# Kernel tuning notes

Measured on AMD Instinct MI355X. Metric: run time of the kernel, lower is better.

Reference implementation:

```python
import jax, jax.numpy as jnp
import numpy as np

N_HEADS, D_MODEL, D_HEAD = 16, 1024, 64
BATCH, SEQ = 2, 2048
INIT_RANGE = 0.02


def setup_inputs() -> dict:
    key = jax.random.key(0)
    ks = jax.random.split(key, 5)
    x = jax.random.normal(ks[0], (BATCH, SEQ, D_MODEL), dtype=jnp.float32)
    W_Q = jax.random.normal(ks[1], (N_HEADS, D_MODEL, D_HEAD), dtype=jnp.float32) * INIT_RANGE
    W_K = jax.random.normal(ks[2], (N_HEADS, D_MODEL, D_HEAD), dtype=jnp.float32) * INIT_RANGE
    W_V = jax.random.normal(ks[3], (N_HEADS, D_MODEL, D_HEAD), dtype=jnp.float32) * INIT_RANGE
    W_O = jax.random.normal(ks[4], (N_HEADS, D_HEAD, D_MODEL), dtype=jnp.float32) * INIT_RANGE
    b_Q = jnp.zeros((N_HEADS, D_HEAD), dtype=jnp.float32)
    b_K = jnp.zeros((N_HEADS, D_HEAD), dtype=jnp.float32)
    b_V = jnp.zeros((N_HEADS, D_HEAD), dtype=jnp.float32)
    b_O = jnp.zeros((D_MODEL,), dtype=jnp.float32)
    return {"normalized_resid_pre": x, "W_Q": W_Q, "W_K": W_K, "W_V": W_V,
            "W_O": W_O, "b_Q": b_Q, "b_K": b_K, "b_V": b_V, "b_O": b_O}


def reference(normalized_resid_pre, W_Q, W_K, W_V, W_O, b_Q, b_K, b_V, b_O):
    x = normalized_resid_pre  # [b, s, d_model]
    q = jnp.einsum('bsm,hmd->bshd', x, W_Q) + b_Q  # [b, s, h, d_head]
    k = jnp.einsum('bsm,hmd->bshd', x, W_K) + b_K
    v = jnp.einsum('bsm,hmd->bshd', x, W_V) + b_V
    scores = jnp.einsum('bqhd,bkhd->bhqk', q, k) / jnp.sqrt(jnp.float32(D_HEAD))
    seq = x.shape[1]
    causal = jnp.tril(jnp.ones((seq, seq), dtype=bool))  # True where allowed
    scores = jnp.where(causal, scores, jnp.float32(-jnp.inf))
    pattern = jax.nn.softmax(scores, axis=-1)  # [b, h, q, k]
    z = jnp.einsum('bhqk,bkhd->bqhd', pattern, v)
    attn_out = jnp.einsum('bqhd,hdm->bqm', z, W_O) + b_O
    return attn_out
```

## Files before the change

kernel.cpp:

```cpp
#include <hip/hip_runtime.h>
#include <hip/hip_bf16.h>

#define BATCH 2
#define SEQL 2048
#define NH 16
#define DH 64
#define DM 1024
#define LDK 72
#define QSCALE 0.1803368801111244f

typedef __hip_bfloat16 bf16;
typedef __attribute__((ext_vector_type(8))) short  bf16x8;
typedef __attribute__((ext_vector_type(4))) float  f32x4;

__device__ __forceinline__ void gl_lds16(const void* g, void* l) {
    __builtin_amdgcn_global_load_lds(
        (const __attribute__((address_space(1))) unsigned int*)g,
        (__attribute__((address_space(3))) unsigned int*)l, 16, 0, 0);
}

__global__ __launch_bounds__(256) void prep_kernel(
    const float* __restrict__ x,
    const float* __restrict__ Wq, const float* __restrict__ Wk,
    const float* __restrict__ Wv, const float* __restrict__ Wo,
    bf16* __restrict__ Wt, bf16* __restrict__ xb)
{
    const int zi = blockIdx.z;
    if (zi == 4) {
        const int bid = blockIdx.y * 16 + blockIdx.x;
        const size_t base = ((size_t)bid * 256 + threadIdx.x) * 4;
        #pragma unroll
        for (int it = 0; it < 16; ++it) {
            const size_t i = base + (size_t)it * 262144;
            const float4 v = *(const float4*)(x + i);
            bf16 o[4];
            o[0] = __float2bfloat16(v.x); o[1] = __float2bfloat16(v.y);
            o[2] = __float2bfloat16(v.z); o[3] = __float2bfloat16(v.w);
            *(uint2*)(xb + i) = *(const uint2*)o;
        }
        return;
    }

    __shared__ float ts[64][65];
    const float* src = (zi == 0) ? Wq : (zi == 1) ? Wk : (zi == 2) ? Wv : Wo;
    bf16* dst = Wt + (size_t)zi * DM * DM;
    const int row0 = blockIdx.y * 64;
    const int col0 = blockIdx.x * 64;
    const int tx = threadIdx.x & 63;
    const int ty = threadIdx.x >> 6;

    if (zi < 3) {
        const int h = col0 >> 6;
        #pragma unroll
        for (int i = 0; i < 16; ++i) {
            const int r = ty + 4 * i;
            ts[r][tx] = src[h * (DM * DH) + (row0 + r) * DH + tx];
        }
    } else {
        #pragma unroll
        for (int i = 0; i < 16; ++i) {
            const int r = ty + 4 * i;
            ts[r][tx] = src[(size_t)(row0 + r) * DM + col0 + tx];
        }
    }
    __syncthreads();
    #pragma unroll
    for (int i = 0; i < 16; ++i) {
        const int rr = ty + 4 * i;
        dst[(size_t)(col0 + rr) * DM + row0 + tx] = __float2bfloat16(ts[tx][rr]);
    }
}

__global__ __launch_bounds__(256) void qkv_gemm(
    const bf16* __restrict__ xb, const bf16* __restrict__ Wt,
    const float* __restrict__ bq, const float* __restrict__ bk, const float* __restrict__ bv,
    bf16* __restrict__ qkv)
{
    __shared__ __align__(16) bf16 As[2][128 * 32];
    __shared__ __align__(16) bf16 Bs[2][128 * 32];

    const int t = threadIdx.x;
    const int lane = t & 63, w = t >> 6;
    const int ml = lane & 15, quad = lane >> 4;
    const int wr = w >> 1, wc = w & 1;
    const int bn = blockIdx.x, bm = blockIdx.y, which = blockIdx.z;

    const bf16* A0 = xb + (size_t)(bm * 128) * DM;
    const bf16* B0 = Wt + (size_t)which * DM * DM + (size_t)(bn * 128) * DM;
    const float* bias = (which == 0) ? bq : (which == 1) ? bk : bv;
    bf16* outb = qkv + (size_t)which * (BATCH * SEQL * NH * DH);
    const float oscale = (which == 0) ? QSCALE : 1.0f;

    f32x4 acc[4][4];
    #pragma unroll
    for (int i = 0; i < 4; ++i)
        #pragma unroll
        for (int j = 0; j < 4; ++j) acc[i][j] = (f32x4){0.f, 0.f, 0.f, 0.f};

    const int r0 = t >> 2, c0 = (t & 3) * 8;
    const int f1 = t + 256;
    const int r1 = f1 >> 2, c1 = (f1 & 3) * 8;

    for (int kt = 0; kt < DM / 64; ++kt) {
        const int k0 = kt * 64;
        __syncthreads();
        #pragma unroll
        for (int half = 0; half < 2; ++half) {
            const int kh = k0 + half * 32;
            gl_lds16(A0 + (size_t)r0 * DM + kh + c0, &As[half][t * 8]);
            gl_lds16(A0 + (size_t)r1 * DM + kh + c1, &As[half][f1 * 8]);
            gl_lds16(B0 + (size_t)r0 * DM + kh + c0, &Bs[half][t * 8]);
            gl_lds16(B0 + (size_t)r1 * DM + kh + c1, &Bs[half][f1 * 8]);
        }
        __syncthreads();
        #pragma unroll
        for (int half = 0; half < 2; ++half) {
            bf16x8 af[4], bfr[4];
            #pragma unroll
            for (int i = 0; i < 4; ++i)
                af[i] = *(const bf16x8*)&As[half][(wr * 64 + i * 16 + ml) * 32 + quad * 8];
            #pragma unroll
            for (int j = 0; j < 4; ++j)
                bfr[j] = *(const bf16x8*)&Bs[half][(wc * 64 + j * 16 + ml) * 32 + quad * 8];
            #pragma unroll
            for (int i = 0; i < 4; ++i)
                #pragma unroll
                for (int j = 0; j < 4; ++j)
                    acc[i][j] = __builtin_amdgcn_mfma_f32_16x16x32_bf16(af[i], bfr[j], acc[i][j], 0, 0, 0);
        }
    }

    float bb[4];
    #pragma unroll
    for (int j = 0; j < 4; ++j) bb[j] = bias[bn * 128 + wc * 64 + j * 16 + ml];

    if (which == 2) {
        #pragma unroll
        for (int i = 0; i < 4; ++i) {
            const int row0v = bm * 128 + wr * 64 + i * 16 + quad * 4;
            const int b = row0v >> 11;
            const int s0 = row0v & (SEQL - 1);
            #pragma unroll
            for (int j = 0; j < 4; ++j) {
                const int col = bn * 128 + wc * 64 + j * 16 + ml;
                const int h = col >> 6, d = col & 63;
                bf16 tmp[4];
                #pragma unroll
                for (int rg = 0; rg < 4; ++rg)
                    tmp[rg] = __float2bfloat16(acc[i][j][rg] + bb[j]);
                *(uint2*)&outb[(((size_t)(b * NH + h)) * DH + d) * SEQL + s0] =
                    *(const uint2*)tmp;
            }
        }
    } else {
        #pragma unroll
        for (int i = 0; i < 4; ++i) {
            #pragma unroll
            for (int rg = 0; rg < 4; ++rg) {
                const int row = bm * 128 + wr * 64 + i * 16 + quad * 4 + rg;
                const int b = row >> 11;
                const int s = row & (SEQL - 1);
                #pragma unroll
                for (int j = 0; j < 4; ++j) {
                    const int col = bn * 128 + wc * 64 + j * 16 + ml;
                    const int h = col >> 6, d = col & 63;
                    outb[(((size_t)(b * NH + h)) * SEQL + s) * DH + d] =
                        __float2bfloat16((acc[i][j][rg] + bb[j]) * oscale);
                }
            }
        }
    }
}

__global__ __launch_bounds__(256) void oproj_gemm(
    const bf16* __restrict__ zb, const bf16* __restrict__ Bt,
    const float* __restrict__ bo, float* __restrict__ out)
{
    __shared__ __align__(16) bf16 As[2][128 * 32];
    __shared__ __align__(16) bf16 Bs[2][64 * 32];

    const int t = threadIdx.x;
    const int lane = t & 63, w = t >> 6;
    const int ml = lane & 15, quad = lane >> 4;
    const int wr = w >> 1, wc = w & 1;
    const int bn = blockIdx.x, bm = blockIdx.y;

    const bf16* A0 = zb + (size_t)(bm * 128) * DM;
    const bf16* B0 = Bt + (size_t)(bn * 64) * DM;

    f32x4 acc[4][2];
    #pragma unroll
    for (int i = 0; i < 4; ++i)
        #pragma unroll
        for (int j = 0; j < 2; ++j) acc[i][j] = (f32x4){0.f, 0.f, 0.f, 0.f};

    const int r0 = t >> 2, c0 = (t & 3) * 8;
    const int f1 = t + 256;
    const int r1 = f1 >> 2, c1 = (f1 & 3) * 8;

    for (int kt = 0; kt < DM / 64; ++kt) {
        const int k0 = kt * 64;
        __syncthreads();
        #pragma unroll
        for (int half = 0; half < 2; ++half) {
            const int kh = k0 + half * 32;
            gl_lds16(A0 + (size_t)r0 * DM + kh + c0, &As[half][t * 8]);
            gl_lds16(A0 + (size_t)r1 * DM + kh + c1, &As[half][f1 * 8]);
            gl_lds16(B0 + (size_t)r0 * DM + kh + c0, &Bs[half][t * 8]);
        }
        __syncthreads();
        #pragma unroll
        for (int half = 0; half < 2; ++half) {
            bf16x8 af[4], bfr[2];
            #pragma unroll
            for (int i = 0; i < 4; ++i)
                af[i] = *(const bf16x8*)&As[half][(wr * 64 + i * 16 + ml) * 32 + quad * 8];
            #pragma unroll
            for (int j = 0; j < 2; ++j)
                bfr[j] = *(const bf16x8*)&Bs[half][(wc * 32 + j * 16 + ml) * 32 + quad * 8];
            #pragma unroll
            for (int i = 0; i < 4; ++i)
                #pragma unroll
                for (int j = 0; j < 2; ++j)
                    acc[i][j] = __builtin_amdgcn_mfma_f32_16x16x32_bf16(af[i], bfr[j], acc[i][j], 0, 0, 0);
        }
    }

    float bb[2];
    #pragma unroll
    for (int j = 0; j < 2; ++j) bb[j] = bo[bn * 64 + wc * 32 + j * 16 + ml];

    #pragma unroll
    for (int i = 0; i < 4; ++i) {
        #pragma unroll
        for (int rg = 0; rg < 4; ++rg) {
            const int row = bm * 128 + wr * 64 + i * 16 + quad * 4 + rg;
            #pragma unroll
            for (int j = 0; j < 2; ++j) {
                const int col = bn * 64 + wc * 32 + j * 16 + ml;
                out[(size_t)row * DM + col] = acc[i][j][rg] + bb[j];
            }
        }
    }
}

__global__ __launch_bounds__(256) void attn_kernel(
    const bf16* __restrict__ qg, const bf16* __restrict__ kg, const bf16* __restrict__ vtg,
    bf16* __restrict__ z)
{
    __shared__ __align__(16) bf16 KsS[2][64 * 64];
    __shared__ __align__(16) bf16 VtS[2][64 * 64];
    __shared__ bf16 PsS[4][16 * LDK];

    const int t    = threadIdx.x;
    const int lane = t & 63;
    const int w    = t >> 6;
    const int m    = lane & 15;
    const int quad = lane >> 4;

    const int bh = blockIdx.x;
    const int b  = bh >> 4;
    const int h  = bh & 15;
    const int qt = (gridDim.y - 1) - blockIdx.y;
    const int q0 = qt * 64;

    const size_t base   = (size_t)bh * SEQL * DH;
    const size_t vtbase = (size_t)bh * DH * SEQL;

    const int s0 = w * 128 + lane;
    const int s1 = s0 + 64;
    const int r0s = s0 >> 3, c0s = (s0 & 7) ^ (r0s & 7);
    const int r1s = s1 >> 3, c1s = (s1 & 7) ^ (r1s & 7);

    bf16x8 aq[2];
    {
        const bf16* qp = qg + base + (size_t)(q0 + w * 16 + m) * DH + quad * 8;
        aq[0] = *(const bf16x8*)(qp);
        aq[1] = *(const bf16x8*)(qp + 32);
    }

    const short ob = (m == 0) ? (short)0x3F80 : (short)0;
    const bf16x8 bones = {ob, ob, ob, ob, ob, ob, ob, ob};

    f32x4 zacc[4];
    #pragma unroll
    for (int nt = 0; nt < 4; ++nt) zacc[nt] = (f32x4){0.f, 0.f, 0.f, 0.f};
    f32x4 lacc = (f32x4){0.f, 0.f, 0.f, 0.f};

    bf16* Psw = PsS[w];

    {
        gl_lds16(kg + base + (size_t)r0s * DH + c0s * 8, &KsS[0][s0 * 8]);
        gl_lds16(kg + base + (size_t)r1s * DH + c1s * 8, &KsS[0][s1 * 8]);
        gl_lds16(vtg + vtbase + (size_t)r0s * SEQL + c0s * 8, &VtS[0][s0 * 8]);
        gl_lds16(vtg + vtbase + (size_t)r1s * SEQL + c1s * 8, &VtS[0][s1 * 8]);
    }

    for (int kt = 0; kt <= qt; ++kt) {
        const int cur = kt & 1;
        __syncthreads();

        if (kt < qt) {
            const int kc = (kt + 1) * 64;
            bf16* Kd = &KsS[cur ^ 1][0];
            bf16* Vd = &VtS[cur ^ 1][0];
            gl_lds16(kg + base + (size_t)(kc + r0s) * DH + c0s * 8, Kd + s0 * 8);
            gl_lds16(kg + base + (size_t)(kc + r1s) * DH + c1s * 8, Kd + s1 * 8);
            gl_lds16(vtg + vtbase + (size_t)r0s * SEQL + kc + c0s * 8, Vd + s0 * 8);
            gl_lds16(vtg + vtbase + (size_t)r1s * SEQL + kc + c1s * 8, Vd + s1 * 8);
        }

        const bf16* Ks = &KsS[cur][0];
        const bf16* Vt = &VtS[cur][0];

        f32x4 sc[4];
        #pragma unroll
        for (int nt = 0; nt < 4; ++nt) sc[nt] = (f32x4){0.f, 0.f, 0.f, 0.f};
        __builtin_amdgcn_s_setprio(1);
        #pragma unroll
        for (int ks = 0; ks < 2; ++ks) {
            #pragma unroll
            for (int nt = 0; nt < 4; ++nt) {
                const int row = nt * 16 + m;
                const int pc  = ((ks << 2) + quad) ^ (m & 7);
                const bf16x8 bk = *(const bf16x8*)(&Ks[row * 64 + pc * 8]);
                sc[nt] = __builtin_amdgcn_mfma_f32_16x16x32_bf16(aq[ks], bk, sc[nt], 0, 0, 0);
            }
        }
        __builtin_amdgcn_s_setprio(0);
        if (kt == qt) {
            #pragma unroll
            for (int nt = 0; nt < 4; ++nt) {
                const int col = nt * 16 + m;
                #pragma unroll
                for (int rg = 0; rg < 4; ++rg) {
                    const int row = w * 16 + quad * 4 + rg;
                    if (col > row) sc[nt][rg] = -1e30f;
                }
            }
        }

        #pragma unroll
        for (int nt = 0; nt < 4; ++nt)
            #pragma unroll
            for (int rg = 0; rg < 4; ++rg)
                Psw[(quad * 4 + rg) * LDK + nt * 16 + m] =
                    __float2bfloat16(__builtin_exp2f(sc[nt][rg]));

        __builtin_amdgcn_s_setprio(1);
        #pragma unroll
        for (int ks = 0; ks < 2; ++ks) {
            const bf16x8 ap = *(const bf16x8*)(&Psw[m * LDK + ks * 32 + quad * 8]);
            lacc = __builtin_amdgcn_mfma_f32_16x16x32_bf16(ap, bones, lacc, 0, 0, 0);
            #pragma unroll
            for (int nt = 0; nt < 4; ++nt) {
                const int row = nt * 16 + m;
                const int pc  = ((ks << 2) + quad) ^ (m & 7);
                const bf16x8 bv = *(const bf16x8*)(&Vt[row * 64 + pc * 8]);
                zacc[nt] = __builtin_amdgcn_mfma_f32_16x16x32_bf16(ap, bv, zacc[nt], 0, 0, 0);
            }
        }
        __builtin_amdgcn_s_setprio(0);
    }

    float invl[4];
    #pragma unroll
    for (int rg = 0; rg < 4; ++rg)
        invl[rg] = 1.f / __shfl(lacc[rg], quad * 16);
    #pragma unroll
    for (int nt = 0; nt < 4; ++nt) {
        const int d = nt * 16 + m;
        #pragma unroll
        for (int rg = 0; rg < 4; ++rg) {
            const int qrow = q0 + w * 16 + quad * 4 + rg;
            z[(((size_t)b * SEQL + qrow) * NH + h) * DH + d] =
                __float2bfloat16(zacc[nt][rg] * invl[rg]);
        }
    }
}

extern "C" void kernel_launch(void* const* d_in, const int* in_sizes, int n_in,
                              void* d_out, int out_size, void* d_ws, size_t ws_size,
                              hipStream_t stream)
{
    const float* x  = (const float*)d_in[0];
    const float* Wq = (const float*)d_in[1];
    const float* Wk = (const float*)d_in[2];
    const float* Wv = (const float*)d_in[3];
    const float* Wo = (const float*)d_in[4];
    const float* bq = (const float*)d_in[5];
    const float* bk = (const float*)d_in[6];
    const float* bv = (const float*)d_in[7];
    const float* bo = (const float*)d_in[8];
    float* out = (float*)d_out;

    const size_t TOK = (size_t)BATCH * SEQL;
    const size_t QKV = TOK * DM;
    bf16* xb  = (bf16*)d_ws;
    bf16* Wt  = xb + QKV;
    bf16* qkv = Wt + 4 * (size_t)DM * DM;
    bf16* zb  = qkv + 3 * QKV;

    prep_kernel<<<dim3(16, 16, 5), 256, 0, stream>>>(x, Wq, Wk, Wv, Wo, Wt, xb);
    qkv_gemm<<<dim3(8, 32, 3), 256, 0, stream>>>(xb, Wt, bq, bk, bv, qkv);
    attn_kernel<<<dim3(BATCH * NH, SEQL / 64), 256, 0, stream>>>(
        qkv, qkv + QKV, qkv + 2 * QKV, zb);
    oproj_gemm<<<dim3(16, 32), 256, 0, stream>>>(zb, Wt + 3 * (size_t)DM * DM, bo, out);
}
```

Before: 185.1 us.

## Restructure attention to 32x32 MFMA with split-KV warps and register-resident P

Rewrites the attention kernel to use 32x32x16 MFMAs, computing S transposed (K x Q) so the probabilities stay in registers and are exchanged across half-waves with shuffles instead of a round trip through LDS. The four waves now split into two query groups and two KV halves, and the KV-half partial outputs are merged through shared memory at the end. The row sum is accumulated in scalar adds instead of an extra MFMA against a ones vector, and the fully masked diagonal quarter is skipped. This aims to cut LDS traffic and MFMA count, at the cost of an extra reduction step, more registers, and skewed per-wave work on the diagonal tile.

```diff
diff --git a/kernel.cpp b/kernel.cpp
--- a/kernel.cpp
+++ b/kernel.cpp
@@ -6,17 +6,23 @@
 #define NH 16
 #define DH 64
 #define DM 1024
-#define LDK 72
 #define QSCALE 0.1803368801111244f
 
 typedef __hip_bfloat16 bf16;
-typedef __attribute__((ext_vector_type(8))) short  bf16x8;
-typedef __attribute__((ext_vector_type(4))) float  f32x4;
+typedef __attribute__((ext_vector_type(8)))  short bf16x8;
+typedef __attribute__((ext_vector_type(4)))  float f32x4;
+typedef __attribute__((ext_vector_type(16))) float f32x16;
 
 __device__ __forceinline__ void gl_lds16(const void* g, void* l) {
     __builtin_amdgcn_global_load_lds(
         (const __attribute__((address_space(1))) unsigned int*)g,
         (__attribute__((address_space(3))) unsigned int*)l, 16, 0, 0);
+}
+
+__device__ __forceinline__ unsigned int pkbf(float a, float b) {
+    union { bf16 h[2]; unsigned int u; } x;
+    x.h[0] = __float2bfloat16(a); x.h[1] = __float2bfloat16(b);
+    return x.u;
 }
 
 __global__ __launch_bounds__(256) void prep_kernel(
@@ -250,13 +256,14 @@
 {
     __shared__ __align__(16) bf16 KsS[2][64 * 64];
     __shared__ __align__(16) bf16 VtS[2][64 * 64];
-    __shared__ bf16 PsS[4][16 * LDK];
 
     const int t    = threadIdx.x;
     const int lane = t & 63;
     const int w    = t >> 6;
-    const int m    = lane & 15;
-    const int quad = lane >> 4;
+    const int q5   = lane & 31;
+    const int hl   = lane >> 5;
+    const int qgr  = w & 1;
+    const int kvg  = w >> 1;
 
     const int bh = blockIdx.x;
     const int b  = bh >> 4;
@@ -267,34 +274,29 @@
     const size_t base   = (size_t)bh * SEQL * DH;
     const size_t vtbase = (size_t)bh * DH * SEQL;
 
-    const int s0 = w * 128 + lane;
-    const int s1 = s0 + 64;
+    const int s0 = t, s1 = t + 256;
     const int r0s = s0 >> 3, c0s = (s0 & 7) ^ (r0s & 7);
     const int r1s = s1 >> 3, c1s = (s1 & 7) ^ (r1s & 7);
 
-    bf16x8 aq[2];
+    bf16x8 aq[4];
     {
-        const bf16* qp = qg + base + (size_t)(q0 + w * 16 + m) * DH + quad * 8;
-        aq[0] = *(const bf16x8*)(qp);
-        aq[1] = *(const bf16x8*)(qp + 32);
-    }
-
-    const short ob = (m == 0) ? (short)0x3F80 : (short)0;
-    const bf16x8 bones = {ob, ob, ob, ob, ob, ob, ob, ob};
-
-    f32x4 zacc[4];
-    #pragma unroll
-    for (int nt = 0; nt < 4; ++nt) zacc[nt] = (f32x4){0.f, 0.f, 0.f, 0.f};
-    f32x4 lacc = (f32x4){0.f, 0.f, 0.f, 0.f};
-
-    bf16* Psw = PsS[w];
-
-    {
-        gl_lds16(kg + base + (size_t)r0s * DH + c0s * 8, &KsS[0][s0 * 8]);
-        gl_lds16(kg + base + (size_t)r1s * DH + c1s * 8, &KsS[0][s1 * 8]);
-        gl_lds16(vtg + vtbase + (size_t)r0s * SEQL + c0s * 8, &VtS[0][s0 * 8]);
-        gl_lds16(vtg + vtbase + (size_t)r1s * SEQL + c1s * 8, &VtS[0][s1 * 8]);
-    }
+        const bf16* qp = qg + base + (size_t)(q0 + qgr * 32 + q5) * DH;
+        #pragma unroll
+        for (int c = 0; c < 4; ++c)
+            aq[c] = *(const bf16x8*)(qp + c * 16 + hl * 8);
+    }
+
+    f32x16 zacc[2];
+    #pragma unroll
+    for (int dg = 0; dg < 2; ++dg)
+        #pragma unroll
+        for (int r = 0; r < 16; ++r) zacc[dg][r] = 0.f;
+    float lacc = 0.f;
+
+    gl_lds16(kg + base + (size_t)r0s * DH + c0s * 8, &KsS[0][s0 * 8]);
+    gl_lds16(kg + base + (size_t)r1s * DH + c1s * 8, &KsS[0][s1 * 8]);
+    gl_lds16(vtg + vtbase + (size_t)r0s * SEQL + c0s * 8, &VtS[0][s0 * 8]);
+    gl_lds16(vtg + vtbase + (size_t)r1s * SEQL + c1s * 8, &VtS[0][s1 * 8]);
 
     for (int kt = 0; kt <= qt; ++kt) {
         const int cur = kt & 1;
@@ -310,71 +312,111 @@
             gl_lds16(vtg + vtbase + (size_t)r1s * SEQL + kc + c1s * 8, Vd + s1 * 8);
         }
 
+        if (kt == qt && kvg == 1 && qgr == 0) continue;
+
         const bf16* Ks = &KsS[cur][0];
         const bf16* Vt = &VtS[cur][0];
 
-        f32x4 sc[4];
-        #pragma unroll
-        for (int nt = 0; nt < 4; ++nt) sc[nt] = (f32x4){0.f, 0.f, 0.f, 0.f};
+        f32x16 sc;
+        #pragma unroll
+        for (int r = 0; r < 16; ++r) sc[r] = 0.f;
+        {
+            const int row = kvg * 32 + q5;
+            const int rx  = row & 7;
+            __builtin_amdgcn_s_setprio(1);
+            #pragma unroll
+            for (int s = 0; s < 4; ++s) {
+                const int cc = (s * 2 + hl) ^ rx;
+                const bf16x8 ak = *(const bf16x8*)(&Ks[row * 64 + cc * 8]);
+                sc = __builtin_amdgcn_mfma_f32_32x32x16_bf16(ak, aq[s], sc, 0, 0, 0);
+            }
+            __builtin_amdgcn_s_setprio(0);
+        }
+
+        if (kt == qt && kvg == qgr) {
+            #pragma unroll
+            for (int r = 0; r < 16; ++r) {
+                const int kvloc = (r & 3) + 8 * (r >> 2) + 4 * hl;
+                sc[r] = (kvloc > q5) ? -1e30f : sc[r];
+            }
+        }
+
+        unsigned int wpk[8];
+        #pragma unroll
+        for (int g = 0; g < 4; ++g) {
+            const float p0 = __builtin_exp2f(sc[4 * g + 0]);
+            const float p1 = __builtin_exp2f(sc[4 * g + 1]);
+            const float p2 = __builtin_exp2f(sc[4 * g + 2]);
+            const float p3 = __builtin_exp2f(sc[4 * g + 3]);
+            lacc += (p0 + p1) + (p2 + p3);
+            wpk[2 * g + 0] = pkbf(p0, p1);
+            wpk[2 * g + 1] = pkbf(p2, p3);
+        }
+
+        bf16x8 pf[2];
+        #pragma unroll
+        for (int ks = 0; ks < 2; ++ks) {
+            const unsigned int S0 = hl ? wpk[4 * ks + 0] : wpk[4 * ks + 2];
+            const unsigned int S1 = hl ? wpk[4 * ks + 1] : wpk[4 * ks + 3];
+            const unsigned int R0 = __shfl_xor((int)S0, 32);
+            const unsigned int R1 = __shfl_xor((int)S1, 32);
+            union { unsigned int u[4]; bf16x8 v; } f;
+            f.u[0] = hl ? R0 : wpk[4 * ks + 0];
+            f.u[1] = hl ? R1 : wpk[4 * ks + 1];
+            f.u[2] = hl ? wpk[4 * ks + 2] : R0;
+            f.u[3] = hl ? wpk[4 * ks + 3] : R1;
+            pf[ks] = f.v;
+        }
+
         __builtin_amdgcn_s_setprio(1);
         #pragma unroll
-        for (int ks = 0; ks < 2; ++ks) {
-            #pragma unroll
-            for (int nt = 0; nt < 4; ++nt) {
-                const int row = nt * 16 + m;
-                const int pc  = ((ks << 2) + quad) ^ (m & 7);
-                const bf16x8 bk = *(const bf16x8*)(&Ks[row * 64 + pc * 8]);
-                sc[nt] = __builtin_amdgcn_mfma_f32_16x16x32_bf16(aq[ks], bk, sc[nt], 0, 0, 0);
+        for (int dg = 0; dg < 2; ++dg) {
+            const int row = dg * 32 + q5;
+            const int rx  = row & 7;
+            #pragma unroll
+            for (int ks = 0; ks < 2; ++ks) {
+                const int cc = (kvg * 4 + ks * 2 + hl) ^ rx;
+                const bf16x8 av = *(const bf16x8*)(&Vt[row * 64 + cc * 8]);
+                zacc[dg] = __builtin_amdgcn_mfma_f32_32x32x16_bf16(av, pf[ks], zacc[dg], 0, 0, 0);
             }
         }
         __builtin_amdgcn_s_setprio(0);
-        if (kt == qt) {
-            #pragma unroll
-            for (int nt = 0; nt < 4; ++nt) {
-                const int col = nt * 16 + m;
+    }
+
+    __syncthreads();
+    if (kvg == 1) {
+        float* sp = (qgr == 0) ? (float*)KsS : (float*)VtS;
+        #pragma unroll
+        for (int dg = 0; dg < 2; ++dg)
+            #pragma unroll
+            for (int r = 0; r < 16; ++r)
+                sp[(dg * 16 + r) * 64 + lane] = zacc[dg][r];
+        sp[2048 + lane] = lacc;
+    }
+    __syncthreads();
+    if (kvg == 0) {
+        const float* sp = (qgr == 0) ? (const float*)KsS : (const float*)VtS;
+        #pragma unroll
+        for (int dg = 0; dg < 2; ++dg)
+            #pragma unroll
+            for (int r = 0; r < 16; ++r)
+                zacc[dg][r] += sp[(dg * 16 + r) * 64 + lane];
+        lacc += sp[2048 + lane];
+        lacc += __shfl_xor(lacc, 32);
+        const float invl = 1.f / lacc;
+
+        const int qrow = q0 + qgr * 32 + q5;
+        bf16* zp = z + (((size_t)b * SEQL + qrow) * NH + h) * DH;
+        #pragma unroll
+        for (int dg = 0; dg < 2; ++dg) {
+            #pragma unroll
+            for (int g2 = 0; g2 < 4; ++g2) {
+                bf16 tmp[4];
                 #pragma unroll
-                for (int rg = 0; rg < 4; ++rg) {
-                    const int row = w * 16 + quad * 4 + rg;
-                    if (col > row) sc[nt][rg] = -1e30f;
-                }
-            }
-        }
-
-        #pragma unroll
-        for (int nt = 0; nt < 4; ++nt)
-            #pragma unroll
-            for (int rg = 0; rg < 4; ++rg)
-                Psw[(quad * 4 + rg) * LDK + nt * 16 + m] =
-                    __float2bfloat16(__builtin_exp2f(sc[nt][rg]));
-
-        __builtin_amdgcn_s_setprio(1);
-        #pragma unroll
-        for (int ks = 0; ks < 2; ++ks) {
-            const bf16x8 ap = *(const bf16x8*)(&Psw[m * LDK + ks * 32 + quad * 8]);
-            lacc = __builtin_amdgcn_mfma_f32_16x16x32_bf16(ap, bones, lacc, 0, 0, 0);
-            #pragma unroll
-            for (int nt = 0; nt < 4; ++nt) {
-                const int row = nt * 16 + m;
-                const int pc  = ((ks << 2) + quad) ^ (m & 7);
-                const bf16x8 bv = *(const bf16x8*)(&Vt[row * 64 + pc * 8]);
-                zacc[nt] = __builtin_amdgcn_mfma_f32_16x16x32_bf16(ap, bv, zacc[nt], 0, 0, 0);
-            }
-        }
-        __builtin_amdgcn_s_setprio(0);
-    }
-
-    float invl[4];
-    #pragma unroll
-    for (int rg = 0; rg < 4; ++rg)
-        invl[rg] = 1.f / __shfl(lacc[rg], quad * 16);
-    #pragma unroll
-    for (int nt = 0; nt < 4; ++nt) {
-        const int d = nt * 16 + m;
-        #pragma unroll
-        for (int rg = 0; rg < 4; ++rg) {
-            const int qrow = q0 + w * 16 + quad * 4 + rg;
-            z[(((size_t)b * SEQL + qrow) * NH + h) * DH + d] =
-                __float2bfloat16(zacc[nt][rg] * invl[rg]);
+                for (int j = 0; j < 4; ++j)
+                    tmp[j] = __float2bfloat16(zacc[dg][4 * g2 + j] * invl);
+                *(uint2*)(zp + dg * 32 + 8 * g2 + 4 * hl) = *(const uint2*)tmp;
+            }
         }
     }
 }
```

Measured after the change: 183.3 us. Within noise of the previous version (-0.9%).
